# Kernel optimization log

Measured on AMD Instinct MI355X. Metric: run time of the kernel, lower is better.

Reference implementation:

```python
import jax, jax.numpy as jnp
import numpy as np

B, T, C, H = 8, 1024, 1536, 12
D = C // H  # head_size = 128
EPS = 1e-5


def layer_norm(x, g, b):
    m = jnp.mean(x, axis=-1, keepdims=True)
    v = jnp.var(x, axis=-1, keepdims=True)
    return (x - m) / jnp.sqrt(v + EPS) * g + b


def batch_norm_T(x, g, b):
    # BatchNorm1d(block_size) on (B, T, C): channels are the T axis;
    # training-mode batch statistics over (B, C), biased variance.
    m = jnp.mean(x, axis=(0, 2), keepdims=True)
    v = jnp.var(x, axis=(0, 2), keepdims=True)
    return (x - m) / jnp.sqrt(v + EPS) * g[None, :, None] + b[None, :, None]


def setup_inputs() -> dict:
    key = jax.random.key(0)
    ks = jax.random.split(key, 12)
    s = 0.02
    inp = {
        "x": jax.random.normal(ks[0], (B, T, C), dtype=jnp.float32),
        # per-head q/k/v projections stacked: (H, C, D)
        "wq": jax.random.normal(ks[1], (H, C, D), dtype=jnp.float32) * s,
        "wk": jax.random.normal(ks[2], (H, C, D), dtype=jnp.float32) * s,
        "wv": jax.random.normal(ks[3], (H, C, D), dtype=jnp.float32) * s,
        "wo": jax.random.normal(ks[4], (C, C), dtype=jnp.float32) * s,
        "bo": jnp.zeros((C,), dtype=jnp.float32),
        "ln1_g": jnp.ones((C,), dtype=jnp.float32),
        "ln1_b": jnp.zeros((C,), dtype=jnp.float32),
        "ln2_g": jnp.ones((C,), dtype=jnp.float32),
        "ln2_b": jnp.zeros((C,), dtype=jnp.float32),
        "w1": jax.random.normal(ks[5], (C, 4 * C), dtype=jnp.float32) * s,
        "b1": jnp.zeros((4 * C,), dtype=jnp.float32),
        "w2": jax.random.normal(ks[6], (4 * C, C), dtype=jnp.float32) * s,
        "b2": jnp.zeros((C,), dtype=jnp.float32),
        "bn1_g": jnp.ones((T,), dtype=jnp.float32),
        "bn1_b": jnp.zeros((T,), dtype=jnp.float32),
        "bn2_g": jnp.ones((T,), dtype=jnp.float32),
        "bn2_b": jnp.zeros((T,), dtype=jnp.float32),
    }
    return inp


def reference(x, wq, wk, wv, wo, bo, ln1_g, ln1_b, ln2_g, ln2_b,
              w1, b1, w2, b2, bn1_g, bn1_b, bn2_g, bn2_b):
    # --- multi-head causal self-attention (pre-LN) ---
    h = layer_norm(x, ln1_g, ln1_b)                       # (B,T,C)
    q = jnp.einsum('btc,hcd->bhtd', h, wq)
    k = jnp.einsum('btc,hcd->bhtd', h, wk)
    v = jnp.einsum('btc,hcd->bhtd', h, wv)
    scores = jnp.einsum('bhtd,bhsd->bhts', q, k) * (D ** -0.5)
    causal = jnp.tril(jnp.ones((T, T), dtype=bool))
    scores = jnp.where(causal, scores, -jnp.inf)
    attn = jax.nn.softmax(scores, axis=-1)                # dropout = identity (eval)
    o = jnp.einsum('bhts,bhsd->bthd', attn, v).reshape(B, T, C)
    sa = o @ wo + bo
    x = x + sa
    x = batch_norm_T(x, bn1_g, bn1_b)
    # --- feed-forward ---
    h2 = layer_norm(x, ln2_g, ln2_b)
    ff = jax.nn.relu(h2 @ w1 + b1) @ w2 + b2
    x = batch_norm_T(x + ff, bn2_g, bn2_b)
    return x
```

## Files before the change

### kernel.cpp

```cpp
#include <hip/hip_runtime.h>
#include <hip/hip_bf16.h>

constexpr int BATCH = 8;
constexpr int SEQ   = 1024;
constexpr int CH    = 1536;
constexpr int NH    = 12;
constexpr int HD    = 128;
constexpr int FFDIM = 6144;
constexpr int NROWS = BATCH * SEQ;
constexpr int QKVLD = 3 * CH;
constexpr float EPS = 1e-5f;

typedef unsigned short ushort;
typedef __attribute__((ext_vector_type(8))) ushort us8;
typedef __attribute__((ext_vector_type(8))) __bf16 bf16x8;
typedef __attribute__((ext_vector_type(4))) float f32x4;

__device__ __forceinline__ float b2f(ushort u) {
  return __uint_as_float(((unsigned)u) << 16);
}
__device__ __forceinline__ ushort f2b(float f) {
  __hip_bfloat16 h = __float2bfloat16(f);
  return *reinterpret_cast<ushort*>(&h);
}

__device__ __forceinline__ void g2l16(const ushort* g, ushort* l) {
  __builtin_amdgcn_global_load_lds(
      (const __attribute__((address_space(1))) void*)g,
      (__attribute__((address_space(3))) void*)l, 16, 0, 0);
}

__device__ __forceinline__ float block_sum(float v, float* red) {
#pragma unroll
  for (int o = 32; o > 0; o >>= 1) v += __shfl_down(v, o, 64);
  const int w = threadIdx.x >> 6;
  if ((threadIdx.x & 63) == 0) red[w] = v;
  __syncthreads();
  const float r = red[0] + red[1] + red[2] + red[3];
  __syncthreads();
  return r;
}

__global__ __launch_bounds__(256) void ln_bf16(const float* __restrict__ x,
                                               const float* __restrict__ g,
                                               const float* __restrict__ b,
                                               ushort* __restrict__ out) {
  __shared__ float row[CH];
  __shared__ float red[4];
  const size_t base = (size_t)blockIdx.x * CH;
  float s = 0.f;
  for (int c = threadIdx.x; c < CH; c += 256) {
    const float v = x[base + c];
    row[c] = v;
    s += v;
  }
  const float mean = block_sum(s, red) * (1.0f / CH);
  float s2 = 0.f;
  for (int c = threadIdx.x; c < CH; c += 256) {
    const float d = row[c] - mean;
    s2 += d * d;
  }
  const float var = block_sum(s2, red) * (1.0f / CH);
  const float rstd = rsqrtf(var + EPS);
  for (int c = threadIdx.x; c < CH; c += 256)
    out[base + c] = f2b((row[c] - mean) * rstd * g[c] + b[c]);
}

__global__ __launch_bounds__(256) void transpose_cast(const float* __restrict__ src,
                                                      ushort* __restrict__ dst,
                                                      int R, int Cc, int ldd,
                                                      long srcZ, long dstZ) {
  __shared__ float tile[32][33];
  src += (size_t)blockIdx.z * srcZ;
  dst += (size_t)blockIdx.z * dstZ;
  const int c0 = blockIdx.x * 32, r0 = blockIdx.y * 32;
  const int tx = threadIdx.x & 31, ty = threadIdx.x >> 5;
#pragma unroll
  for (int i = ty; i < 32; i += 8)
    tile[i][tx] = src[(size_t)(r0 + i) * Cc + c0 + tx];
  __syncthreads();
#pragma unroll
  for (int i = ty; i < 32; i += 8)
    dst[(size_t)(c0 + i) * ldd + r0 + tx] = f2b(tile[tx][i]);
}

constexpr int BT = 128;
constexpr int BK = 32;

template <int RELU, int BIAS, int RES, int OUTBF>
__global__ __launch_bounds__(256) void gemm_bf16(
    const ushort* __restrict__ A, int lda,
    const ushort* __restrict__ Bt, int ldb,
    void* __restrict__ Cm, int ldc,
    const float* __restrict__ bias,
    const float* __restrict__ res, int ldr,
    int K) {
  __shared__ ushort As[BT * BK];
  __shared__ ushort Bs[BT * BK];
  const int tid = threadIdx.x;
  const int lane = tid & 63;
  const int wv = tid >> 6;
  const int m0 = blockIdx.y * BT;
  const int n0 = blockIdx.x * BT;
  const int srow = wv * 32 + (lane >> 2);
  const int schunk = (lane & 3) * 8;
  const ushort* gA0 = A + (size_t)(m0 + srow) * lda + schunk;
  const ushort* gA1 = gA0 + (size_t)16 * lda;
  const ushort* gB0 = Bt + (size_t)(n0 + srow) * ldb + schunk;
  const ushort* gB1 = gB0 + (size_t)16 * ldb;
  ushort* lA0 = As + (wv * 32) * BK;
  ushort* lA1 = lA0 + 16 * BK;
  ushort* lB0 = Bs + (wv * 32) * BK;
  ushort* lB1 = lB0 + 16 * BK;
  const int wm = (wv >> 1) * 64, wn = (wv & 1) * 64;
  const int fr = lane & 15;
  const int quad = lane >> 4;
  const int koff = quad * 8;

  f32x4 acc[4][4] = {{}};
  for (int k0 = 0; k0 < K; k0 += BK) {
    __syncthreads();
    g2l16(gA0 + k0, lA0);
    g2l16(gA1 + k0, lA1);
    g2l16(gB0 + k0, lB0);
    g2l16(gB1 + k0, lB1);
    __syncthreads();
    bf16x8 af[4], bf[4];
#pragma unroll
    for (int mi = 0; mi < 4; ++mi)
      af[mi] = *(const bf16x8*)&As[(wm + mi * 16 + fr) * BK + koff];
#pragma unroll
    for (int ni = 0; ni < 4; ++ni)
      bf[ni] = *(const bf16x8*)&Bs[(wn + ni * 16 + fr) * BK + koff];
#pragma unroll
    for (int mi = 0; mi < 4; ++mi)
#pragma unroll
      for (int ni = 0; ni < 4; ++ni)
        acc[mi][ni] = __builtin_amdgcn_mfma_f32_16x16x32_bf16(af[mi], bf[ni], acc[mi][ni], 0, 0, 0);
  }
#pragma unroll
  for (int ni = 0; ni < 4; ++ni) {
    const int col = n0 + wn + ni * 16 + fr;
    const float bs = BIAS ? bias[col] : 0.f;
#pragma unroll
    for (int mi = 0; mi < 4; ++mi) {
      const int rowb = m0 + wm + mi * 16 + quad * 4;
#pragma unroll
      for (int r = 0; r < 4; ++r) {
        float v = acc[mi][ni][r] + bs;
        if (RELU) v = fmaxf(v, 0.f);
        const size_t idx = (size_t)(rowb + r) * ldc + col;
        if (RES) v += res[(size_t)(rowb + r) * ldr + col];
        if (OUTBF) ((ushort*)Cm)[idx] = f2b(v);
        else       ((float*)Cm)[idx] = v;
      }
    }
  }
}

constexpr int FQT = 64;
constexpr int VLD = 72;

__global__ __launch_bounds__(256) void flash_attn_mfma(
    const ushort* __restrict__ q, const ushort* __restrict__ k,
    const ushort* __restrict__ v, ushort* __restrict__ o,
    int ld, int ldo) {
  __shared__ ushort Vt[HD][VLD];
  __shared__ ushort Ps[4][16][VLD];
  const int tid = threadIdx.x;
  const int lane = tid & 63;
  const int w = tid >> 6;
  const int fr = lane & 15;
  const int quad = lane >> 4;
  const int qt = blockIdx.x;
  const int b = blockIdx.y / NH;
  const int h = blockIdx.y % NH;
  const size_t base = (size_t)b * SEQ * ld + (size_t)h * HD;
  const int q0 = qt * FQT;
  const int qrow = q0 + w * 16;
  const float scale = 0.08838834764831845f;

  bf16x8 aq[4];
  {
    const ushort* qp = q + base + (size_t)(qrow + fr) * ld + quad * 8;
#pragma unroll
    for (int ks = 0; ks < 4; ++ks) aq[ks] = *(const bf16x8*)(qp + ks * 32);
  }

  float m_i[4], l_i[4];
  f32x4 oacc[8];
#pragma unroll
  for (int i = 0; i < 4; ++i) { m_i[i] = -3.0e38f; l_i[i] = 0.f; }
#pragma unroll
  for (int n8 = 0; n8 < 8; ++n8) oacc[n8] = (f32x4){0.f, 0.f, 0.f, 0.f};

  for (int jt = 0; jt <= qt; ++jt) {
    const int j0 = jt * FQT;
    f32x4 sacc[4];
#pragma unroll
    for (int ni = 0; ni < 4; ++ni) sacc[ni] = (f32x4){0.f, 0.f, 0.f, 0.f};
#pragma unroll
    for (int ks = 0; ks < 4; ++ks) {
      const ushort* kp = k + base + (size_t)(j0 + fr) * ld + ks * 32 + quad * 8;
#pragma unroll
      for (int ni = 0; ni < 4; ++ni) {
        const bf16x8 kf = *(const bf16x8*)(kp + (size_t)(ni * 16) * ld);
        sacc[ni] = __builtin_amdgcn_mfma_f32_16x16x32_bf16(aq[ks], kf, sacc[ni], 0, 0, 0);
      }
    }
    const bool diag = (jt == qt);
    float alpha[4];
#pragma unroll
    for (int i = 0; i < 4; ++i) {
      const int qg = qrow + quad * 4 + i;
      float pv[4];
      float vmax = -3.0e38f;
#pragma unroll
      for (int ni = 0; ni < 4; ++ni) {
        float sv = sacc[ni][i] * scale;
        if (diag && (j0 + ni * 16 + fr > qg)) sv = -3.0e38f;
        pv[ni] = sv;
        vmax = fmaxf(vmax, sv);
      }
#pragma unroll
      for (int mm = 8; mm >= 1; mm >>= 1) vmax = fmaxf(vmax, __shfl_xor(vmax, mm, 64));
      const float m_new = fmaxf(m_i[i], vmax);
      alpha[i] = __expf(m_i[i] - m_new);
      m_i[i] = m_new;
      float rsum = 0.f;
#pragma unroll
      for (int ni = 0; ni < 4; ++ni) {
        const float pe = __expf(pv[ni] - m_new);
        Ps[w][quad * 4 + i][ni * 16 + fr] = f2b(pe);
        rsum += pe;
      }
#pragma unroll
      for (int mm = 8; mm >= 1; mm >>= 1) rsum += __shfl_xor(rsum, mm, 64);
      l_i[i] = l_i[i] * alpha[i] + rsum;
#pragma unroll
      for (int n8 = 0; n8 < 8; ++n8) oacc[n8][i] *= alpha[i];
    }
    __syncthreads();
#pragma unroll
    for (int rep = 0; rep < 4; ++rep) {
      const int c = tid + rep * 256;
      const int j = c & 63;
      const int dc = c >> 6;
      const us8 vv = *(const us8*)(v + base + (size_t)(j0 + j) * ld + dc * 8);
#pragma unroll
      for (int ii = 0; ii < 8; ++ii) Vt[dc * 8 + ii][j] = vv[ii];
    }
    __syncthreads();
#pragma unroll
    for (int js = 0; js < 2; ++js) {
      const bf16x8 pf = *(const bf16x8*)&Ps[w][fr][js * 32 + quad * 8];
#pragma unroll
      for (int n8 = 0; n8 < 8; ++n8) {
        const bf16x8 vf = *(const bf16x8*)&Vt[n8 * 16 + fr][js * 32 + quad * 8];
        oacc[n8] = __builtin_amdgcn_mfma_f32_16x16x32_bf16(pf, vf, oacc[n8], 0, 0, 0);
      }
    }
  }
#pragma unroll
  for (int i = 0; i < 4; ++i) {
    const float inv = 1.0f / l_i[i];
    ushort* op = o + ((size_t)b * SEQ + qrow + quad * 4 + i) * ldo + (size_t)h * HD;
#pragma unroll
    for (int n8 = 0; n8 < 8; ++n8) op[n8 * 16 + fr] = f2b(oacc[n8][i] * inv);
  }
}

__global__ __launch_bounds__(256) void bn_stats(const float* __restrict__ x,
                                                float* __restrict__ mean,
                                                float* __restrict__ rstd) {
  __shared__ float red[4];
  const int t = blockIdx.x;
  float s = 0.f;
  for (int bb = 0; bb < BATCH; ++bb) {
    const float* p = x + ((size_t)bb * SEQ + t) * CH;
    for (int c = threadIdx.x; c < CH; c += 256) s += p[c];
  }
  const float m = block_sum(s, red) * (1.0f / (BATCH * CH));
  float s2 = 0.f;
  for (int bb = 0; bb < BATCH; ++bb) {
    const float* p = x + ((size_t)bb * SEQ + t) * CH;
    for (int c = threadIdx.x; c < CH; c += 256) {
      const float d = p[c] - m;
      s2 += d * d;
    }
  }
  const float var = block_sum(s2, red) * (1.0f / (BATCH * CH));
  if (threadIdx.x == 0) {
    mean[t] = m;
    rstd[t] = rsqrtf(var + EPS);
  }
}

__global__ __launch_bounds__(256) void bn_apply(const float* __restrict__ x,
                                                float* __restrict__ out,
                                                const float* __restrict__ mean,
                                                const float* __restrict__ rstd,
                                                const float* __restrict__ g,
                                                const float* __restrict__ bb) {
  const size_t i = (size_t)blockIdx.x * 256 + threadIdx.x;
  const int t = (int)((i / CH) % SEQ);
  out[i] = (x[i] - mean[t]) * rstd[t] * g[t] + bb[t];
}

extern "C" void kernel_launch(void* const* d_in, const int* in_sizes, int n_in,
                              void* d_out, int out_size, void* d_ws, size_t ws_size,
                              hipStream_t stream) {
  const float* x    = (const float*)d_in[0];
  const float* wq   = (const float*)d_in[1];
  const float* wk   = (const float*)d_in[2];
  const float* wv   = (const float*)d_in[3];
  const float* wo   = (const float*)d_in[4];
  const float* bo   = (const float*)d_in[5];
  const float* ln1g = (const float*)d_in[6];
  const float* ln1b = (const float*)d_in[7];
  const float* ln2g = (const float*)d_in[8];
  const float* ln2b = (const float*)d_in[9];
  const float* w1   = (const float*)d_in[10];
  const float* b1   = (const float*)d_in[11];
  const float* w2   = (const float*)d_in[12];
  const float* b2   = (const float*)d_in[13];
  const float* bn1g = (const float*)d_in[14];
  const float* bn1b = (const float*)d_in[15];
  const float* bn2g = (const float*)d_in[16];
  const float* bn2b = (const float*)d_in[17];
  float* out = (float*)d_out;

  ushort* wsu = (ushort*)d_ws;
  const size_t NCs   = (size_t)NROWS * CH;
  ushort* R0    = wsu;
  ushort* QKV   = wsu + NCs;
  ushort* wqkvT = wsu + NCs + (size_t)NROWS * QKVLD;
  ushort* woT   = wqkvT + (size_t)QKVLD * CH;
  float*  meanp = (float*)(woT + (size_t)CH * CH);
  float*  rstdp = meanp + SEQ;
  ushort* w1T   = QKV;
  ushort* w2T   = QKV + (size_t)FFDIM * CH;
  ushort* FF1   = QKV + 2 * (size_t)FFDIM * CH;

  const dim3 blk(256);

  transpose_cast<<<dim3(HD / 32, CH / 32, NH), blk, 0, stream>>>(
      wq, wqkvT, CH, HD, CH, (long)CH * HD, (long)HD * CH);
  transpose_cast<<<dim3(HD / 32, CH / 32, NH), blk, 0, stream>>>(
      wk, wqkvT + (size_t)CH * CH, CH, HD, CH, (long)CH * HD, (long)HD * CH);
  transpose_cast<<<dim3(HD / 32, CH / 32, NH), blk, 0, stream>>>(
      wv, wqkvT + 2 * (size_t)CH * CH, CH, HD, CH, (long)CH * HD, (long)HD * CH);
  transpose_cast<<<dim3(CH / 32, CH / 32, 1), blk, 0, stream>>>(
      wo, woT, CH, CH, CH, 0, 0);

  ln_bf16<<<NROWS, blk, 0, stream>>>(x, ln1g, ln1b, R0);

  gemm_bf16<0, 0, 0, 1><<<dim3(QKVLD / BT, NROWS / BT), blk, 0, stream>>>(
      R0, CH, wqkvT, CH, QKV, QKVLD, nullptr, nullptr, 0, CH);

  flash_attn_mfma<<<dim3(SEQ / FQT, BATCH * NH), blk, 0, stream>>>(
      QKV, QKV + CH, QKV + 2 * CH, R0, QKVLD, CH);

  transpose_cast<<<dim3(FFDIM / 32, CH / 32, 1), blk, 0, stream>>>(
      w1, w1T, CH, FFDIM, CH, 0, 0);
  transpose_cast<<<dim3(CH / 32, FFDIM / 32, 1), blk, 0, stream>>>(
      w2, w2T, FFDIM, CH, FFDIM, 0, 0);

  gemm_bf16<0, 1, 1, 0><<<dim3(CH / BT, NROWS / BT), blk, 0, stream>>>(
      R0, CH, woT, CH, out, CH, bo, x, CH, CH);

  bn_stats<<<SEQ, blk, 0, stream>>>(out, meanp, rstdp);
  bn_apply<<<(NROWS * CH) / 256, blk, 0, stream>>>(out, out, meanp, rstdp, bn1g, bn1b);

  ln_bf16<<<NROWS, blk, 0, stream>>>(out, ln2g, ln2b, R0);

  constexpr int FFC = 4096;
  for (int c = 0; c < NROWS / FFC; ++c) {
    const size_t r0 = (size_t)c * FFC;
    gemm_bf16<1, 1, 0, 1><<<dim3(FFDIM / BT, FFC / BT), blk, 0, stream>>>(
        R0 + r0 * CH, CH, w1T, CH, FF1, FFDIM, b1, nullptr, 0, CH);
    gemm_bf16<0, 1, 1, 0><<<dim3(CH / BT, FFC / BT), blk, 0, stream>>>(
        FF1, FFDIM, w2T, FFDIM, out + r0 * CH, CH, b2, out + r0 * CH, CH, FFDIM);
  }

  bn_stats<<<SEQ, blk, 0, stream>>>(out, meanp, rstdp);
  bn_apply<<<(NROWS * CH) / 256, blk, 0, stream>>>(out, out, meanp, rstdp, bn2g, bn2b);
}
```

Baseline: 1.375 ms.

## Pre-transpose V per head and feed attention MFMA directly from global

A new kernel writes V for each (batch, head) into a transposed buffer before attention. The attention kernel then loads V^T fragments straight from global memory and drops the per-tile LDS transpose and its two __syncthreads. Attention output is written into the Q slot of the QKV buffer, and the output-projection GEMM reads it from there with the QKV stride. The cost is an extra transpose pass over V and strided global loads inside the MFMA loop, which lean on cache reuse across waves.

```diff
diff --git a/kernel.cpp b/kernel.cpp
--- a/kernel.cpp
+++ b/kernel.cpp
@@ -82,6 +82,24 @@
 #pragma unroll
   for (int i = ty; i < 32; i += 8)
     dst[(size_t)(c0 + i) * ldd + r0 + tx] = f2b(tile[tx][i]);
+}
+
+__global__ __launch_bounds__(256) void transpose_v(const ushort* __restrict__ src,
+                                                   ushort* __restrict__ dst) {
+  __shared__ ushort tile[32][33];
+  const int bh = blockIdx.z;
+  const int b = bh / NH, h = bh % NH;
+  const ushort* s = src + (size_t)b * SEQ * QKVLD + (size_t)h * HD;
+  ushort* d = dst + (size_t)bh * HD * SEQ;
+  const int t0 = blockIdx.x * 32, d0 = blockIdx.y * 32;
+  const int tx = threadIdx.x & 31, ty = threadIdx.x >> 5;
+#pragma unroll
+  for (int i = ty; i < 32; i += 8)
+    tile[i][tx] = s[(size_t)(t0 + i) * QKVLD + d0 + tx];
+  __syncthreads();
+#pragma unroll
+  for (int i = ty; i < 32; i += 8)
+    d[(size_t)(d0 + i) * SEQ + t0 + tx] = tile[tx][i];
 }
 
 constexpr int BT = 128;
@@ -163,9 +181,8 @@
 
 __global__ __launch_bounds__(256) void flash_attn_mfma(
     const ushort* __restrict__ q, const ushort* __restrict__ k,
-    const ushort* __restrict__ v, ushort* __restrict__ o,
+    const ushort* __restrict__ vt, ushort* __restrict__ o,
     int ld, int ldo) {
-  __shared__ ushort Vt[HD][VLD];
   __shared__ ushort Ps[4][16][VLD];
   const int tid = threadIdx.x;
   const int lane = tid & 63;
@@ -176,6 +193,7 @@
   const int b = blockIdx.y / NH;
   const int h = blockIdx.y % NH;
   const size_t base = (size_t)b * SEQ * ld + (size_t)h * HD;
+  const ushort* vtb = vt + (size_t)(b * NH + h) * HD * SEQ;
   const int q0 = qt * FQT;
   const int qrow = q0 + w * 16;
   const float scale = 0.08838834764831845f;
@@ -240,23 +258,13 @@
 #pragma unroll
       for (int n8 = 0; n8 < 8; ++n8) oacc[n8][i] *= alpha[i];
     }
-    __syncthreads();
-#pragma unroll
-    for (int rep = 0; rep < 4; ++rep) {
-      const int c = tid + rep * 256;
-      const int j = c & 63;
-      const int dc = c >> 6;
-      const us8 vv = *(const us8*)(v + base + (size_t)(j0 + j) * ld + dc * 8);
-#pragma unroll
-      for (int ii = 0; ii < 8; ++ii) Vt[dc * 8 + ii][j] = vv[ii];
-    }
-    __syncthreads();
 #pragma unroll
     for (int js = 0; js < 2; ++js) {
       const bf16x8 pf = *(const bf16x8*)&Ps[w][fr][js * 32 + quad * 8];
+      const ushort* vp = vtb + (size_t)fr * SEQ + j0 + js * 32 + quad * 8;
 #pragma unroll
       for (int n8 = 0; n8 < 8; ++n8) {
-        const bf16x8 vf = *(const bf16x8*)&Vt[n8 * 16 + fr][js * 32 + quad * 8];
+        const bf16x8 vf = *(const bf16x8*)(vp + (size_t)(n8 * 16) * SEQ);
         oacc[n8] = __builtin_amdgcn_mfma_f32_16x16x32_bf16(pf, vf, oacc[n8], 0, 0, 0);
       }
     }
@@ -358,16 +366,19 @@
   gemm_bf16<0, 0, 0, 1><<<dim3(QKVLD / BT, NROWS / BT), blk, 0, stream>>>(
       R0, CH, wqkvT, CH, QKV, QKVLD, nullptr, nullptr, 0, CH);
 
+  transpose_v<<<dim3(SEQ / 32, HD / 32, BATCH * NH), blk, 0, stream>>>(
+      QKV + 2 * CH, R0);
+
   flash_attn_mfma<<<dim3(SEQ / FQT, BATCH * NH), blk, 0, stream>>>(
-      QKV, QKV + CH, QKV + 2 * CH, R0, QKVLD, CH);
+      QKV, QKV + CH, R0, QKV, QKVLD, QKVLD);
+
+  gemm_bf16<0, 1, 1, 0><<<dim3(CH / BT, NROWS / BT), blk, 0, stream>>>(
+      QKV, QKVLD, woT, CH, out, CH, bo, x, CH, CH);
 
   transpose_cast<<<dim3(FFDIM / 32, CH / 32, 1), blk, 0, stream>>>(
       w1, w1T, CH, FFDIM, CH, 0, 0);
   transpose_cast<<<dim3(CH / 32, FFDIM / 32, 1), blk, 0, stream>>>(
       w2, w2T, FFDIM, CH, FFDIM, 0, 0);
-
-  gemm_bf16<0, 1, 1, 0><<<dim3(CH / BT, NROWS / BT), blk, 0, stream>>>(
-      R0, CH, woT, CH, out, CH, bo, x, CH, CH);
 
   bn_stats<<<SEQ, blk, 0, stream>>>(out, meanp, rstdp);
   bn_apply<<<(NROWS * CH) / 256, blk, 0, stream>>>(out, out, meanp, rstdp, bn1g, bn1b);
```

After: 1.526 ms. 11.0% more time.
